# Optimization experiments

Measured on AMD Instinct MI355X. Metric: run time of the kernel, lower is better.

## Reference

```python
import jax, jax.numpy as jnp
import numpy as np

BN_EPS = 1e-5


def setup_inputs() -> dict:
    key = jax.random.key(0)
    ks = jax.random.split(key, 10)
    B, C, N = 16, 512, 4096
    Cr = C // 4
    s = 0.05
    return {
        "x": jax.random.normal(ks[0], (B, C, N), dtype=jnp.float32),
        # channel attention MLP (1x1 convs on pooled vector)
        "w1": jax.random.normal(ks[1], (Cr, C), dtype=jnp.float32) * s,
        "b1": jnp.zeros((Cr,), jnp.float32),
        "w2": jax.random.normal(ks[2], (C, Cr), dtype=jnp.float32) * s,
        "b2": jnp.zeros((C,), jnp.float32),
        # spatial attention branch
        "w3": jax.random.normal(ks[3], (Cr, C), dtype=jnp.float32) * s,
        "b3": jnp.zeros((Cr,), jnp.float32),
        "bn_gamma": jnp.ones((Cr,), jnp.float32),
        "bn_beta": jnp.zeros((Cr,), jnp.float32),
        "bn_mean": jnp.zeros((Cr,), jnp.float32),
        "bn_var": jnp.ones((Cr,), jnp.float32),
        "w4": jax.random.normal(ks[4], (1, Cr), dtype=jnp.float32) * s,
        "b4": jnp.zeros((1,), jnp.float32),
    }


def reference(x, w1, b1, w2, b2, w3, b3, bn_gamma, bn_beta, bn_mean, bn_var, w4, b4):
    # x: [B, C, N]; inference semantics (Dropout = identity, BN uses running stats)
    # ---- channel attention ----
    pooled = jnp.mean(x, axis=-1)                        # [B, C] (AdaptiveAvgPool1d(1))
    h = jax.nn.relu(pooled @ w1.T + b1)                  # [B, C/4]
    ca = jax.nn.sigmoid(h @ w2.T + b2)[:, :, None]       # [B, C, 1]
    x_ca = x * ca                                        # [B, C, N]
    # ---- spatial attention ----
    h2 = jnp.einsum('oc,bcn->bon', w3, x_ca) + b3[:, None]    # [B, C/4, N]
    inv = bn_gamma / jnp.sqrt(bn_var + BN_EPS)                 # [C/4]
    h2 = h2 * inv[:, None] + (bn_beta - bn_mean * inv)[:, None]
    h2 = jax.nn.relu(h2)
    sa = jax.nn.sigmoid(jnp.einsum('oc,bcn->bon', w4, h2) + b4[:, None])  # [B, 1, N]
    return x + x_ca * sa
```

## Files before the change

kernel.cpp:

```cpp
#include <hip/hip_runtime.h>
#include <math.h>

constexpr int B  = 16;
constexpr int C  = 512;
constexpr int N  = 4096;
constexpr int CR = 128;
constexpr int NT = 64;
constexpr int KC = 64;

typedef __attribute__((ext_vector_type(8))) short bf16x8;
typedef __attribute__((ext_vector_type(4))) float f32x4;

__device__ __forceinline__ float sigmoidf_(float v) {
    return 1.0f / (1.0f + __expf(-v));
}
__device__ __forceinline__ unsigned f2bf(float f) {
    unsigned u = __float_as_uint(f);
    u += 0x7fffu + ((u >> 16) & 1u);
    return u >> 16;
}

#define LGKM_BARRIER() do {                                   \
    asm volatile("s_waitcnt lgkmcnt(0)" ::: "memory");        \
    __builtin_amdgcn_s_barrier();                             \
    asm volatile("" ::: "memory");                            \
} while (0)

__global__ __launch_bounds__(256) void k_pre(
    const float* __restrict__ x, float* __restrict__ pooled,
    const float* __restrict__ w3, const float* __restrict__ b3,
    const float* __restrict__ gamma, const float* __restrict__ beta,
    const float* __restrict__ mean, const float* __restrict__ var,
    unsigned short* __restrict__ w3s, float* __restrict__ bias2)
{
    if (blockIdx.x < 2048) {
        int w    = threadIdx.x >> 6;
        int lane = threadIdx.x & 63;
        int row  = blockIdx.x * 4 + w;
        const float4* xr = (const float4*)(x + (size_t)row * N);
        float s = 0.f;
        #pragma unroll
        for (int i = 0; i < 16; ++i) {
            float4 v = xr[i * 64 + lane];
            s += v.x + v.y + v.z + v.w;
        }
        #pragma unroll
        for (int off = 32; off; off >>= 1) s += __shfl_xor(s, off, 64);
        if (lane == 0) pooled[row] = s * (1.0f / N);
    } else {
        int idx = (blockIdx.x - 2048) * 256 + threadIdx.x;
        int o  = idx >> 6;
        int g  = idx & 63;
        int ck = g >> 3;
        int c8 = (g & 7) * 8;
        int c  = ck * KC + c8;
        float inv = gamma[o] * rsqrtf(var[o] + 1e-5f);
        float4 a  = *(const float4*)(w3 + o * C + c);
        float4 bq = *(const float4*)(w3 + o * C + c + 4);
        unsigned r0 = f2bf(a.x * inv)  | (f2bf(a.y * inv) << 16);
        unsigned r1 = f2bf(a.z * inv)  | (f2bf(a.w * inv) << 16);
        unsigned r2 = f2bf(bq.x * inv) | (f2bf(bq.y * inv) << 16);
        unsigned r3 = f2bf(bq.z * inv) | (f2bf(bq.w * inv) << 16);
        int byte = (o * 128 + c8 * 2) ^ ((o & 7) << 4);
        *(uint4*)((char*)w3s + ck * 16384 + byte) = make_uint4(r0, r1, r2, r3);
        if (idx < CR) {
            float iv = gamma[idx] * rsqrtf(var[idx] + 1e-5f);
            bias2[idx] = b3[idx] * iv + beta[idx] - mean[idx] * iv;
        }
    }
}

__global__ __launch_bounds__(128) void k_ca(
    const float* __restrict__ pooled,
    const float* __restrict__ w1, const float* __restrict__ b1,
    const float* __restrict__ w2, const float* __restrict__ b2,
    float* __restrict__ ca)
{
    __shared__ float ps[C];
    __shared__ float hs[CR];
    int b = blockIdx.x, t = threadIdx.x;
    #pragma unroll
    for (int i = 0; i < 4; ++i) ps[t + i * 128] = pooled[b * C + t + i * 128];
    __syncthreads();

    float acc = b1[t];
    const float4* wr = (const float4*)(w1 + t * C);
    const float4* pr = (const float4*)ps;
    #pragma unroll 4
    for (int i = 0; i < C / 4; ++i) {
        float4 wv = wr[i], pv = pr[i];
        acc += wv.x * pv.x + wv.y * pv.y + wv.z * pv.z + wv.w * pv.w;
    }
    hs[t] = fmaxf(acc, 0.f);
    __syncthreads();

    #pragma unroll
    for (int k = 0; k < 4; ++k) {
        int c2 = t + k * 128;
        float a = b2[c2];
        const float4* w2r = (const float4*)(w2 + c2 * CR);
        const float4* hr  = (const float4*)hs;
        #pragma unroll 4
        for (int i = 0; i < CR / 4; ++i) {
            float4 wv = w2r[i], hv = hr[i];
            a += wv.x * hv.x + wv.y * hv.y + wv.z * hv.z + wv.w * hv.w;
        }
        ca[b * C + c2] = sigmoidf_(a);
    }
}

__global__ __launch_bounds__(256) void k_main(
    const float* __restrict__ x, const float* __restrict__ ca,
    const unsigned short* __restrict__ w3s, const float* __restrict__ bias2,
    const float* __restrict__ w4, const float* __restrict__ b4,
    float* __restrict__ out)
{
    __shared__ __align__(16) short lds_w[CR * KC];
    __shared__ __align__(16) short lds_x[NT * KC];
    __shared__ float ca_s[C];
    __shared__ __align__(16) float sa_s[NT];
    __shared__ float red[2][NT];
    __shared__ float bias2_s[CR];
    __shared__ float w4_s[CR];

    const int t    = threadIdx.x;
    const int lane = t & 63;
    const int w    = t >> 6;
    const int b    = blockIdx.y;
    const int n0   = blockIdx.x * NT;
    const int wo   = (w & 1) * 64;
    const int wn   = (w >> 1) * 32;

    ca_s[t]       = ca[b * C + t];
    ca_s[t + 256] = ca[b * C + t + 256];
    if (t < CR) { bias2_s[t] = bias2[t]; w4_s[t] = w4[t]; }

    const size_t xbase = (size_t)b * C * N + n0;
    const int ng = t & 31;
    const int cg = t >> 5;

    float2 xv[8];
    uint4  wv[4];

#define LOADX(CK) do { const int c0_ = (CK) * KC;                              \
    _Pragma("unroll") for (int ci = 0; ci < 8; ++ci)                           \
        xv[ci] = *(const float2*)(x + xbase + (size_t)(c0_ + cg * 8 + ci) * N + 2 * ng); \
} while (0)
#define LOADW(CK) do { const char* ws_ = (const char*)w3s + (CK) * 16384;      \
    _Pragma("unroll") for (int i = 0; i < 4; ++i)                              \
        wv[i] = *(const uint4*)(ws_ + i * 4096 + t * 16);                      \
} while (0)

    f32x4 acc[4][2];
    #pragma unroll
    for (int i = 0; i < 4; ++i) { acc[i][0] = (f32x4)0.f; acc[i][1] = (f32x4)0.f; }

    LOADX(0);
    LOADW(0);
    LGKM_BARRIER();

    for (int ck = 0; ck < C / KC; ++ck) {
        const int c0 = ck * KC;
        #pragma unroll
        for (int i = 0; i < 4; ++i)
            *(uint4*)((char*)lds_w + i * 4096 + t * 16) = wv[i];
        {
            unsigned q0[4], q1[4];
            #pragma unroll
            for (int h = 0; h < 4; ++h) {
                float s0 = ca_s[c0 + cg * 8 + 2 * h];
                float s1 = ca_s[c0 + cg * 8 + 2 * h + 1];
                q0[h] = f2bf(xv[2 * h].x * s0) | (f2bf(xv[2 * h + 1].x * s1) << 16);
                q1[h] = f2bf(xv[2 * h].y * s0) | (f2bf(xv[2 * h + 1].y * s1) << 16);
            }
            int nl0 = 2 * ng, nl1 = 2 * ng + 1;
            int a0 = (nl0 * 128 + cg * 16) ^ ((nl0 & 7) << 4);
            int a1 = (nl1 * 128 + cg * 16) ^ ((nl1 & 7) << 4);
            *(uint4*)((char*)lds_x + a0) = make_uint4(q0[0], q0[1], q0[2], q0[3]);
            *(uint4*)((char*)lds_x + a1) = make_uint4(q1[0], q1[1], q1[2], q1[3]);
        }
        if (ck < C / KC - 1) {
            LOADX(ck + 1);
            LOADW(ck + 1);
        }
        LGKM_BARRIER();
        #pragma unroll
        for (int kk = 0; kk < 2; ++kk) {
            bf16x8 af[4], bfr[2];
            #pragma unroll
            for (int i = 0; i < 4; ++i) {
                int ar = wo + i * 16 + (lane & 15);
                int ab = (ar * 128 + kk * 64 + (lane >> 4) * 16) ^ ((ar & 7) << 4);
                af[i] = *(const bf16x8*)((const char*)lds_w + ab);
            }
            #pragma unroll
            for (int j = 0; j < 2; ++j) {
                int br = wn + j * 16 + (lane & 15);
                int bb = (br * 128 + kk * 64 + (lane >> 4) * 16) ^ ((br & 7) << 4);
                bfr[j] = *(const bf16x8*)((const char*)lds_x + bb);
            }
            #pragma unroll
            for (int i = 0; i < 4; ++i)
                #pragma unroll
                for (int j = 0; j < 2; ++j)
                    acc[i][j] = __builtin_amdgcn_mfma_f32_16x16x32_bf16(af[i], bfr[j], acc[i][j], 0, 0, 0);
        }
        LGKM_BARRIER();
    }

    #pragma unroll
    for (int j = 0; j < 2; ++j) {
        float p = 0.f;
        #pragma unroll
        for (int i = 0; i < 4; ++i) {
            #pragma unroll
            for (int r = 0; r < 4; ++r) {
                int o = wo + i * 16 + (lane >> 4) * 4 + r;
                float hval = acc[i][j][r] + bias2_s[o];
                p = fmaf(w4_s[o], fmaxf(hval, 0.f), p);
            }
        }
        p += __shfl_xor(p, 16, 64);
        p += __shfl_xor(p, 32, 64);
        if (lane < 16) red[w & 1][wn + j * 16 + lane] = p;
    }
    __syncthreads();
    if (t < NT) sa_s[t] = sigmoidf_(red[0][t] + red[1][t] + b4[0]);
    __syncthreads();

    #pragma unroll 4
    for (int it = 0; it < 32; ++it) {
        int f4 = it * 256 + t;
        int c  = f4 >> 4;
        int n4 = f4 & 15;
        size_t off = xbase + (size_t)c * N + n4 * 4;
        float4 v = *(const float4*)(x + off);
        float cav = ca_s[c];
        float4 sv = *(const float4*)&sa_s[n4 * 4];
        float4 o4;
        o4.x = v.x * fmaf(cav, sv.x, 1.0f);
        o4.y = v.y * fmaf(cav, sv.y, 1.0f);
        o4.z = v.z * fmaf(cav, sv.z, 1.0f);
        o4.w = v.w * fmaf(cav, sv.w, 1.0f);
        *(float4*)(out + off) = o4;
    }
#undef LOADX
#undef LOADW
}

extern "C" void kernel_launch(void* const* d_in, const int* in_sizes, int n_in,
                              void* d_out, int out_size, void* d_ws, size_t ws_size,
                              hipStream_t stream)
{
    const float* x   = (const float*)d_in[0];
    const float* w1  = (const float*)d_in[1];
    const float* b1  = (const float*)d_in[2];
    const float* w2  = (const float*)d_in[3];
    const float* b2  = (const float*)d_in[4];
    const float* w3  = (const float*)d_in[5];
    const float* b3  = (const float*)d_in[6];
    const float* g   = (const float*)d_in[7];
    const float* be  = (const float*)d_in[8];
    const float* mn  = (const float*)d_in[9];
    const float* vr  = (const float*)d_in[10];
    const float* w4  = (const float*)d_in[11];
    const float* b4  = (const float*)d_in[12];
    float* out = (float*)d_out;

    float* ws     = (float*)d_ws;
    float* pooled = ws;
    float* ca     = ws + 8192;
    float* bias2  = ws + 16384;
    unsigned short* w3s = (unsigned short*)(ws + 16640);

    k_pre<<<2048 + 32, 256, 0, stream>>>(x, pooled, w3, b3, g, be, mn, vr, w3s, bias2);
    k_ca<<<B, 128, 0, stream>>>(pooled, w1, b1, w2, b2, ca);
    dim3 g3(N / NT, B);
    k_main<<<g3, 256, 0, stream>>>(x, ca, w3s, bias2, w4, b4, out);
}
```

Measured before the change: 141.0 us.

## Load weights as pre-swizzled MFMA fragments and double-buffer x tile in LDS

The prep kernel now writes the scaled bf16 w3 weights directly in the per-lane MFMA fragment order. The main kernel therefore loads A fragments straight from global memory (L2-resident) into registers instead of staging them through LDS. The x tile gets a two-slot LDS buffer with two register prefetch sets, which removes one barrier per K-chunk and overlaps conversion of the next chunk with MFMA on the current one. A launch bound of two blocks per CU is added. The trade-off is more VGPR pressure and repeated global weight reads per block.

Result: faster. 119.9 us (-14.9%).

```diff
diff --git a/kernel.cpp b/kernel.cpp
--- a/kernel.cpp
+++ b/kernel.cpp
@@ -31,7 +31,7 @@
     const float* __restrict__ w3, const float* __restrict__ b3,
     const float* __restrict__ gamma, const float* __restrict__ beta,
     const float* __restrict__ mean, const float* __restrict__ var,
-    unsigned short* __restrict__ w3s, float* __restrict__ bias2)
+    unsigned short* __restrict__ w3f, float* __restrict__ bias2)
 {
     if (blockIdx.x < 2048) {
         int w    = threadIdx.x >> 6;
@@ -48,12 +48,14 @@
         for (int off = 32; off; off >>= 1) s += __shfl_xor(s, off, 64);
         if (lane == 0) pooled[row] = s * (1.0f / N);
     } else {
-        int idx = (blockIdx.x - 2048) * 256 + threadIdx.x;
-        int o  = idx >> 6;
-        int g  = idx & 63;
-        int ck = g >> 3;
-        int c8 = (g & 7) * 8;
-        int c  = ck * KC + c8;
+        int idx  = (blockIdx.x - 2048) * 256 + threadIdx.x;
+        int g    = idx >> 6;
+        int lane = idx & 63;
+        int ck   = g >> 4;
+        int kk   = (g >> 3) & 1;
+        int ob   = g & 7;
+        int o    = ob * 16 + (lane & 15);
+        int c    = ck * 64 + kk * 32 + (lane >> 4) * 8;
         float inv = gamma[o] * rsqrtf(var[o] + 1e-5f);
         float4 a  = *(const float4*)(w3 + o * C + c);
         float4 bq = *(const float4*)(w3 + o * C + c + 4);
@@ -61,8 +63,7 @@
         unsigned r1 = f2bf(a.z * inv)  | (f2bf(a.w * inv) << 16);
         unsigned r2 = f2bf(bq.x * inv) | (f2bf(bq.y * inv) << 16);
         unsigned r3 = f2bf(bq.z * inv) | (f2bf(bq.w * inv) << 16);
-        int byte = (o * 128 + c8 * 2) ^ ((o & 7) << 4);
-        *(uint4*)((char*)w3s + ck * 16384 + byte) = make_uint4(r0, r1, r2, r3);
+        *(uint4*)((char*)w3f + (size_t)idx * 16) = make_uint4(r0, r1, r2, r3);
         if (idx < CR) {
             float iv = gamma[idx] * rsqrtf(var[idx] + 1e-5f);
             bias2[idx] = b3[idx] * iv + beta[idx] - mean[idx] * iv;
@@ -109,14 +110,13 @@
     }
 }
 
-__global__ __launch_bounds__(256) void k_main(
+__global__ __launch_bounds__(256, 2) void k_main(
     const float* __restrict__ x, const float* __restrict__ ca,
-    const unsigned short* __restrict__ w3s, const float* __restrict__ bias2,
+    const unsigned short* __restrict__ w3f, const float* __restrict__ bias2,
     const float* __restrict__ w4, const float* __restrict__ b4,
     float* __restrict__ out)
 {
-    __shared__ __align__(16) short lds_w[CR * KC];
-    __shared__ __align__(16) short lds_x[NT * KC];
+    __shared__ __align__(16) short lds_x[2][NT * KC];
     __shared__ float ca_s[C];
     __shared__ __align__(16) float sa_s[NT];
     __shared__ float red[2][NT];
@@ -130,82 +130,80 @@
     const int n0   = blockIdx.x * NT;
     const int wo   = (w & 1) * 64;
     const int wn   = (w >> 1) * 32;
+    const int ob0  = wo >> 4;
+
+    const size_t xbase = (size_t)b * C * N + n0;
+    const int ng = t & 31;
+    const int cg = t >> 5;
+
+    float2 xva[8], xvb[8];
+
+#define LOADX(dst, CK) do { const int c0_ = (CK) * KC;                         \
+    _Pragma("unroll") for (int ci = 0; ci < 8; ++ci)                           \
+        dst[ci] = *(const float2*)(x + xbase + (size_t)(c0_ + cg * 8 + ci) * N + 2 * ng); \
+} while (0)
+
+#define CONVERT_WRITE(src, CK, BUF) do { const int c0_ = (CK) * KC;            \
+    unsigned q0[4], q1[4];                                                     \
+    _Pragma("unroll") for (int h = 0; h < 4; ++h) {                            \
+        float s0 = ca_s[c0_ + cg * 8 + 2 * h];                                 \
+        float s1 = ca_s[c0_ + cg * 8 + 2 * h + 1];                             \
+        q0[h] = f2bf(src[2 * h].x * s0) | (f2bf(src[2 * h + 1].x * s1) << 16); \
+        q1[h] = f2bf(src[2 * h].y * s0) | (f2bf(src[2 * h + 1].y * s1) << 16); \
+    }                                                                          \
+    int nl0 = 2 * ng, nl1 = 2 * ng + 1;                                        \
+    int a0 = (nl0 * 128 + cg * 16) ^ ((nl0 & 7) << 4);                         \
+    int a1 = (nl1 * 128 + cg * 16) ^ ((nl1 & 7) << 4);                         \
+    *(uint4*)((char*)lds_x[BUF] + a0) = make_uint4(q0[0], q0[1], q0[2], q0[3]);\
+    *(uint4*)((char*)lds_x[BUF] + a1) = make_uint4(q1[0], q1[1], q1[2], q1[3]);\
+} while (0)
+
+    LOADX(xva, 0);
+    LOADX(xvb, 1);
 
     ca_s[t]       = ca[b * C + t];
     ca_s[t + 256] = ca[b * C + t + 256];
     if (t < CR) { bias2_s[t] = bias2[t]; w4_s[t] = w4[t]; }
-
-    const size_t xbase = (size_t)b * C * N + n0;
-    const int ng = t & 31;
-    const int cg = t >> 5;
-
-    float2 xv[8];
-    uint4  wv[4];
-
-#define LOADX(CK) do { const int c0_ = (CK) * KC;                              \
-    _Pragma("unroll") for (int ci = 0; ci < 8; ++ci)                           \
-        xv[ci] = *(const float2*)(x + xbase + (size_t)(c0_ + cg * 8 + ci) * N + 2 * ng); \
-} while (0)
-#define LOADW(CK) do { const char* ws_ = (const char*)w3s + (CK) * 16384;      \
-    _Pragma("unroll") for (int i = 0; i < 4; ++i)                              \
-        wv[i] = *(const uint4*)(ws_ + i * 4096 + t * 16);                      \
-} while (0)
+    LGKM_BARRIER();
+
+    CONVERT_WRITE(xva, 0, 0);
 
     f32x4 acc[4][2];
     #pragma unroll
     for (int i = 0; i < 4; ++i) { acc[i][0] = (f32x4)0.f; acc[i][1] = (f32x4)0.f; }
 
-    LOADX(0);
-    LOADW(0);
-    LGKM_BARRIER();
-
-    for (int ck = 0; ck < C / KC; ++ck) {
-        const int c0 = ck * KC;
-        #pragma unroll
-        for (int i = 0; i < 4; ++i)
-            *(uint4*)((char*)lds_w + i * 4096 + t * 16) = wv[i];
-        {
-            unsigned q0[4], q1[4];
-            #pragma unroll
-            for (int h = 0; h < 4; ++h) {
-                float s0 = ca_s[c0 + cg * 8 + 2 * h];
-                float s1 = ca_s[c0 + cg * 8 + 2 * h + 1];
-                q0[h] = f2bf(xv[2 * h].x * s0) | (f2bf(xv[2 * h + 1].x * s1) << 16);
-                q1[h] = f2bf(xv[2 * h].y * s0) | (f2bf(xv[2 * h + 1].y * s1) << 16);
+    const char* wf = (const char*)w3f;
+
+    #pragma unroll
+    for (int ck = 0; ck < 8; ++ck) {
+        bf16x8 af[2][4];
+        #pragma unroll
+        for (int kk = 0; kk < 2; ++kk)
+            #pragma unroll
+            for (int i = 0; i < 4; ++i) {
+                int g = ck * 16 + kk * 8 + ob0 + i;
+                af[kk][i] = *(const bf16x8*)(wf + (size_t)(g * 64 + lane) * 16);
             }
-            int nl0 = 2 * ng, nl1 = 2 * ng + 1;
-            int a0 = (nl0 * 128 + cg * 16) ^ ((nl0 & 7) << 4);
-            int a1 = (nl1 * 128 + cg * 16) ^ ((nl1 & 7) << 4);
-            *(uint4*)((char*)lds_x + a0) = make_uint4(q0[0], q0[1], q0[2], q0[3]);
-            *(uint4*)((char*)lds_x + a1) = make_uint4(q1[0], q1[1], q1[2], q1[3]);
-        }
-        if (ck < C / KC - 1) {
-            LOADX(ck + 1);
-            LOADW(ck + 1);
-        }
+        if (ck < 6) { if (ck & 1) LOADX(xvb, ck + 2); else LOADX(xva, ck + 2); }
+
         LGKM_BARRIER();
+
         #pragma unroll
         for (int kk = 0; kk < 2; ++kk) {
-            bf16x8 af[4], bfr[2];
-            #pragma unroll
-            for (int i = 0; i < 4; ++i) {
-                int ar = wo + i * 16 + (lane & 15);
-                int ab = (ar * 128 + kk * 64 + (lane >> 4) * 16) ^ ((ar & 7) << 4);
-                af[i] = *(const bf16x8*)((const char*)lds_w + ab);
-            }
+            bf16x8 bfr[2];
             #pragma unroll
             for (int j = 0; j < 2; ++j) {
                 int br = wn + j * 16 + (lane & 15);
                 int bb = (br * 128 + kk * 64 + (lane >> 4) * 16) ^ ((br & 7) << 4);
-                bfr[j] = *(const bf16x8*)((const char*)lds_x + bb);
+                bfr[j] = *(const bf16x8*)((const char*)lds_x[ck & 1] + bb);
             }
             #pragma unroll
             for (int i = 0; i < 4; ++i)
                 #pragma unroll
                 for (int j = 0; j < 2; ++j)
-                    acc[i][j] = __builtin_amdgcn_mfma_f32_16x16x32_bf16(af[i], bfr[j], acc[i][j], 0, 0, 0);
-        }
-        LGKM_BARRIER();
+                    acc[i][j] = __builtin_amdgcn_mfma_f32_16x16x32_bf16(af[kk][i], bfr[j], acc[i][j], 0, 0, 0);
+        }
+        if (ck < 7) { if (ck & 1) CONVERT_WRITE(xva, ck + 1, 0); else CONVERT_WRITE(xvb, ck + 1, 1); }
     }
 
     #pragma unroll
@@ -245,7 +243,7 @@
         *(float4*)(out + off) = o4;
     }
 #undef LOADX
-#undef LOADW
+#undef CONVERT_WRITE
 }
 
 extern "C" void kernel_launch(void* const* d_in, const int* in_sizes, int n_in,
@@ -271,10 +269,10 @@
     float* pooled = ws;
     float* ca     = ws + 8192;
     float* bias2  = ws + 16384;
-    unsigned short* w3s = (unsigned short*)(ws + 16640);
-
-    k_pre<<<2048 + 32, 256, 0, stream>>>(x, pooled, w3, b3, g, be, mn, vr, w3s, bias2);
+    unsigned short* w3f = (unsigned short*)(ws + 16640);
+
+    k_pre<<<2048 + 32, 256, 0, stream>>>(x, pooled, w3, b3, g, be, mn, vr, w3f, bias2);
     k_ca<<<B, 128, 0, stream>>>(pooled, w1, b1, w2, b2, ca);
     dim3 g3(N / NT, B);
-    k_main<<<g3, 256, 0, stream>>>(x, ca, w3s, bias2, w4, b4, out);
-}
+    k_main<<<g3, 256, 0, stream>>>(x, ca, w3f, bias2, w4, b4, out);
+}
```
